# Kernel tuning notes

Measured on AMD Instinct MI355X. Metric: run time of the kernel, lower is better.

The kernel has to match this reference:

```python
import jax, jax.numpy as jnp
import numpy as np


def setup_inputs() -> dict:
    key = jax.random.key(0)
    k1, k2 = jax.random.split(key)
    B, S, D, K = 16, 4096, 256, 4096
    x = jax.random.normal(k1, (B, S, D), dtype=jnp.float32)
    scale = 1.0 / K  # matches nn.init.uniform_(-scale, scale)
    embeddings = jax.random.uniform(k2, (K, D), dtype=jnp.float32, minval=-scale, maxval=scale)
    return {"x": x, "embeddings": embeddings}


def reference(x, embeddings):
    # Flatten all leading dims: [N, D]
    in_shape = x.shape
    flat = x.reshape(-1, in_shape[-1])
    distances = (
        jnp.sum(flat ** 2, axis=1, keepdims=True)
        + jnp.sum(embeddings ** 2, axis=1)
        - 2.0 * flat @ embeddings.T
    )
    proposal = jnp.argmin(distances, axis=-1).reshape(in_shape[:-1])  # [B, S] int
    quantized = embeddings[proposal]  # [B, S, D] gather
    return quantized, proposal
```

## Files before the change

kernel.cpp:

```cpp
#include <hip/hip_runtime.h>
#include <hip/hip_bf16.h>
#include <stdint.h>

#define NROWS 65536
#define DDIM  256
#define KCAND 4096
#define CAP   48
#define MARGIN1 8e-4f
#define MARGIN2 8e-4f

#define LSTRIDE 132

typedef __bf16 bf16x8 __attribute__((ext_vector_type(8)));
typedef float  f32x4  __attribute__((ext_vector_type(4)));
typedef unsigned int u32;
typedef unsigned long long u64;

__device__ __forceinline__ u32 f2bf_u(float f) {
    u32 u = __float_as_uint(f);
    u += 0x7fffu + ((u >> 16) & 1u);
    return u >> 16;
}
__device__ __forceinline__ u32 pack2(float lo, float hi) { return f2bf_u(lo) | (f2bf_u(hi) << 16); }
__device__ __forceinline__ u32 fkey(float f) {
    u32 u = __float_as_uint(f);
    return (u & 0x80000000u) ? ~u : (u | 0x80000000u);
}
__device__ __forceinline__ float funkey(u32 k) {
    u32 u = (k & 0x80000000u) ? (k ^ 0x80000000u) : ~k;
    return __uint_as_float(u);
}
__device__ __forceinline__ float vmax4(f32x4 v) {
    return fmaxf(fmaxf(v[0], v[1]), fmaxf(v[2], v[3]));
}

__device__ __forceinline__ float exact_r(const float* __restrict__ xr, float A,
                                         const float* __restrict__ er) {
    float b = 0.f, acc = 0.f;
    #pragma unroll 8
    for (int d = 0; d < DDIM; ++d) {
        float e = er[d];
        b   = fmaf(e, e, b);
        acc = fmaf(2.0f * xr[d], e, acc);
    }
    return (A + b) - acc;
}

__launch_bounds__(256)
__global__ void convert_e(const float* __restrict__ e, u32* __restrict__ ebf) {
    int T = blockIdx.x * blockDim.x + threadIdx.x;
    int L = T & 63, u = (T >> 6) & 3, kc = (T >> 8) & 7, s = T >> 11;
    int cand = s * 64 + u * 16 + (L & 15);
    int k0 = kc * 32 + (L >> 4) * 8;
    const float4* src = (const float4*)(e + (size_t)cand * DDIM + k0);
    float4 a = src[0], b = src[1];
    uint4 o;
    o.x = pack2(a.x, a.y); o.y = pack2(a.z, a.w);
    o.z = pack2(b.x, b.y); o.w = pack2(b.z, b.w);
    ((uint4*)ebf)[T] = o;
}

__launch_bounds__(256, 3)
__global__ void phase1(const float* __restrict__ x, const u32* __restrict__ ebf,
                       u32* __restrict__ cnt, uint2* __restrict__ list) {
    __shared__ u32 lxd[64 * LSTRIDE];
    __shared__ u32 rowBestK[64];

    const int tid = threadIdx.x;
    const int rowBase = blockIdx.x * 64;
    if (tid < 64) rowBestK[tid] = 0x007FFFFFu;

    {
        const float4* x4 = (const float4*)(x + (size_t)rowBase * DDIM);
        #pragma unroll
        for (int j = 0; j < 16; ++j) {
            int idx = j * 256 + tid;
            int r = idx >> 6, c4 = idx & 63;
            float4 v = x4[idx];
            *(uint2*)&lxd[r * LSTRIDE + 2 * c4] = make_uint2(pack2(v.x, v.y), pack2(v.z, v.w));
        }
    }
    __syncthreads();

    const int L = tid & 63;
    const int w = __builtin_amdgcn_readfirstlane(tid >> 6);
    const int lq = L >> 4, ln = L & 15;
    const int vL = L << 4;

    const char* ebc_w = (const char*)ebf + (size_t)w * 32768;

    auto loadB = [&](int it_, int kc_, bf16x8* dst) {
        const char* kb = ebc_w + (size_t)it_ * 131072 + kc_ * 4096;
        #pragma unroll
        for (int u = 0; u < 4; ++u)
            dst[u] = *(const bf16x8*)(kb + u * 1024 + vL);
    };

    const char* pa = (const char*)lxd + ln * (LSTRIDE * 4) + lq * 16;

    bf16x8 bb[2][4];
    f32x4 acc[4][4];
    const f32x4 Z4 = {0.f, 0.f, 0.f, 0.f};

    loadB(0, 0, bb[0]);
    #pragma unroll
    for (int kc = 0; kc < 8; ++kc) {
        if (kc < 7) loadB(0, kc + 1, bb[(kc + 1) & 1]);
        bf16x8 fa[4];
        #pragma unroll
        for (int t = 0; t < 4; ++t)
            fa[t] = *(const bf16x8*)(pa + t * (16 * LSTRIDE * 4) + kc * 64);
        #pragma unroll
        for (int a = 0; a < 4; ++a)
            #pragma unroll
            for (int u = 0; u < 4; ++u)
                acc[a][u] = (kc == 0)
                    ? __builtin_amdgcn_mfma_f32_16x16x32_bf16(bb[0][u], fa[a], Z4, 0, 0, 0)
                    : __builtin_amdgcn_mfma_f32_16x16x32_bf16(bb[kc & 1][u], fa[a], acc[a][u], 0, 0, 0);
    }
    #pragma unroll
    for (int a = 0; a < 4; ++a) {
        float lmax = fmaxf(fmaxf(vmax4(acc[a][0]), vmax4(acc[a][1])),
                           fmaxf(vmax4(acc[a][2]), vmax4(acc[a][3])));
        float m = fmaxf(lmax, __shfl_xor(lmax, 16, 64));
        m = fmaxf(m, __shfl_xor(m, 32, 64));
        if (lq == 0) atomicMax(&rowBestK[a * 16 + ln], fkey(m));
    }
    __syncthreads();

    loadB(0, 0, bb[0]);
    #pragma unroll 1
    for (int it = 0; it < 16; ++it) {
        {
            loadB(it, 1, bb[1]);
            bf16x8 fa[4];
            #pragma unroll
            for (int t = 0; t < 4; ++t)
                fa[t] = *(const bf16x8*)(pa + t * (16 * LSTRIDE * 4));
            #pragma unroll
            for (int a = 0; a < 4; ++a)
                #pragma unroll
                for (int u = 0; u < 4; ++u)
                    acc[a][u] = __builtin_amdgcn_mfma_f32_16x16x32_bf16(bb[0][u], fa[a], Z4, 0, 0, 0);
        }
        #pragma unroll
        for (int kc = 1; kc < 8; ++kc) {
            int g = it * 8 + kc;
            if (g < 127) { int gn = g + 1; loadB(gn >> 3, gn & 7, bb[(kc + 1) & 1]); }
            bf16x8 fa[4];
            #pragma unroll
            for (int t = 0; t < 4; ++t)
                fa[t] = *(const bf16x8*)(pa + t * (16 * LSTRIDE * 4) + kc * 64);
            #pragma unroll
            for (int a = 0; a < 4; ++a)
                #pragma unroll
                for (int u = 0; u < 4; ++u)
                    acc[a][u] = __builtin_amdgcn_mfma_f32_16x16x32_bf16(bb[kc & 1][u], fa[a], acc[a][u], 0, 0, 0);
        }

        int strip = it * 4 + w;
        u32 seen[4];
        #pragma unroll
        for (int a = 0; a < 4; ++a) seen[a] = rowBestK[a * 16 + ln];

        #pragma unroll
        for (int a = 0; a < 4; ++a) {
            float lmax = fmaxf(fmaxf(vmax4(acc[a][0]), vmax4(acc[a][1])),
                               fmaxf(vmax4(acc[a][2]), vmax4(acc[a][3])));
            float m = fmaxf(lmax, __shfl_xor(lmax, 16, 64));
            m = fmaxf(m, __shfl_xor(m, 32, 64));
            if (lq == 0) atomicMax(&rowBestK[a * 16 + ln], fkey(m));
            float eff  = fmaxf(m, funkey(seen[a]));
            float thrA = eff - 0.5f * MARGIN1;
            if (__ballot(lmax >= thrA)) {
                int c = 0;
                #pragma unroll
                for (int u = 0; u < 4; ++u)
                    #pragma unroll
                    for (int r = 0; r < 4; ++r)
                        c += (acc[a][u][r] >= thrA) ? 1 : 0;
                int p = c, t;
                t = __shfl_up(p, 16, 64); if (lq >= 1) p += t;
                t = __shfl_up(p, 32, 64); if (lq >= 2) p += t;
                int grow = rowBase + a * 16 + ln;
                u32 base = 0;
                if (lq == 3 && p > 0) base = atomicAdd(&cnt[grow], (u32)p);
                base = __shfl(base, 48 + ln, 64);
                u32 pos = base + (u32)(p - c);
                #pragma unroll
                for (int u = 0; u < 4; ++u)
                    #pragma unroll
                    for (int r = 0; r < 4; ++r) {
                        float av = acc[a][u][r];
                        if (av >= thrA) {
                            if (pos < CAP)
                                list[(size_t)grow * CAP + pos] =
                                    make_uint2(__float_as_uint(-2.f * av),
                                               (u32)(strip * 64 + u * 16 + lq * 4 + r));
                            ++pos;
                        }
                    }
            }
        }
    }
}

__launch_bounds__(256)
__global__ void phase2(const float* __restrict__ x, const float* __restrict__ emb,
                       const u32* __restrict__ cnt, const uint2* __restrict__ list,
                       float* __restrict__ outq, float* __restrict__ outp) {
    __shared__ float xs[4][DDIM];
    const int wid = threadIdx.x >> 6;
    const int row = blockIdx.x * 4 + wid;
    const int L   = threadIdx.x & 63;

    u32 n = cnt[row];
    u32 kstar;

    if (n == 1) {
        kstar = list[(size_t)row * CAP].y;
    } else {
        float4 v = ((const float4*)(x + (size_t)row * DDIM))[L];
        *(float4*)&xs[wid][L * 4] = v;
        double s = (double)v.x * v.x + (double)v.y * v.y + (double)v.z * v.z + (double)v.w * v.w;
        #pragma unroll
        for (int o = 32; o; o >>= 1) s += __shfl_xor(s, o, 64);
        float A = (float)s;

        u64 key = 0xFFFFFFFFFFFFFFFFull;
        if (n <= CAP) {
            float vv = INFINITY; u32 kk = 0;
            if (L < (int)n) { uint2 e = list[(size_t)row * CAP + L]; vv = __uint_as_float(e.x); kk = e.y; }
            float mv = vv;
            #pragma unroll
            for (int o = 32; o; o >>= 1) mv = fminf(mv, __shfl_xor(mv, o, 64));
            if (L < (int)n && vv <= mv + MARGIN2) {
                float r = exact_r(xs[wid], A, emb + (size_t)kk * DDIM);
                key = ((u64)fkey(r) << 32) | (u64)kk;
            }
        } else {
            for (int c = 0; c < KCAND / 64; ++c) {
                u32 k = (u32)(c * 64 + L);
                float r = exact_r(xs[wid], A, emb + (size_t)k * DDIM);
                u64 cand = ((u64)fkey(r) << 32) | (u64)k;
                key = (cand < key) ? cand : key;
            }
        }
        #pragma unroll
        for (int o = 32; o; o >>= 1) {
            u64 other = __shfl_xor(key, o, 64);
            key = (other < key) ? other : key;
        }
        kstar = (u32)(key & 0xFFFFFFFFull);
    }

    float4 q = ((const float4*)(emb + (size_t)kstar * DDIM))[L];
    ((float4*)(outq + (size_t)row * DDIM))[L] = q;
    if (L == 0) outp[row] = (float)kstar;
}

extern "C" void kernel_launch(void* const* d_in, const int* in_sizes, int n_in,
                              void* d_out, int out_size, void* d_ws, size_t ws_size,
                              hipStream_t stream) {
    const float* x   = (const float*)d_in[0];
    const float* emb = (const float*)d_in[1];
    float* outq = (float*)d_out;
    float* outp = outq + (size_t)NROWS * DDIM;

    char* ws = (char*)d_ws;
    u32*   ebf  = (u32*)ws;
    u32*   cnt  = (u32*)(ws + (2u << 20));
    uint2* list = (uint2*)(ws + (3u << 20));

    hipMemsetAsync(cnt, 0, (size_t)NROWS * sizeof(u32), stream);
    convert_e<<<512, 256, 0, stream>>>(emb, ebf);
    phase1<<<NROWS / 64, 256, 0, stream>>>(x, ebf, cnt, list);
    phase2<<<NROWS / 4, 256, 0, stream>>>(x, emb, cnt, list, outq, outp);
}
```

Baseline: 452.4 us.

## Double phase1 row tile to 128 and skip exact rescoring for single survivors

Phase1 now processes 128 rows per block instead of 64, with 8 accumulator tiles per wave, so each bf16 codebook fragment loaded from global memory is reused across twice as many rows. This halves total codebook traffic, at the cost of more registers and LDS and a lower occupancy bound (2 blocks instead of 3). Phase2 now checks whether exactly one candidate survives the margin filter. If so it picks that candidate directly and skips loading x and the exact fp32 rescoring.

```diff
diff --git a/kernel.cpp b/kernel.cpp
--- a/kernel.cpp
+++ b/kernel.cpp
@@ -10,6 +10,7 @@
 #define MARGIN2 8e-4f
 
 #define LSTRIDE 132
+#define ROWS_PB 128
 
 typedef __bf16 bf16x8 __attribute__((ext_vector_type(8)));
 typedef float  f32x4  __attribute__((ext_vector_type(4)));
@@ -60,20 +61,20 @@
     ((uint4*)ebf)[T] = o;
 }
 
-__launch_bounds__(256, 3)
+__launch_bounds__(256, 2)
 __global__ void phase1(const float* __restrict__ x, const u32* __restrict__ ebf,
                        u32* __restrict__ cnt, uint2* __restrict__ list) {
-    __shared__ u32 lxd[64 * LSTRIDE];
-    __shared__ u32 rowBestK[64];
+    __shared__ u32 lxd[ROWS_PB * LSTRIDE];
+    __shared__ u32 rowBestK[ROWS_PB];
 
     const int tid = threadIdx.x;
-    const int rowBase = blockIdx.x * 64;
-    if (tid < 64) rowBestK[tid] = 0x007FFFFFu;
+    const int rowBase = blockIdx.x * ROWS_PB;
+    if (tid < ROWS_PB) rowBestK[tid] = 0x007FFFFFu;
 
     {
         const float4* x4 = (const float4*)(x + (size_t)rowBase * DDIM);
         #pragma unroll
-        for (int j = 0; j < 16; ++j) {
+        for (int j = 0; j < 32; ++j) {
             int idx = j * 256 + tid;
             int r = idx >> 6, c4 = idx & 63;
             float4 v = x4[idx];
@@ -99,27 +100,25 @@
     const char* pa = (const char*)lxd + ln * (LSTRIDE * 4) + lq * 16;
 
     bf16x8 bb[2][4];
-    f32x4 acc[4][4];
+    f32x4 acc[8][4];
     const f32x4 Z4 = {0.f, 0.f, 0.f, 0.f};
 
     loadB(0, 0, bb[0]);
     #pragma unroll
     for (int kc = 0; kc < 8; ++kc) {
         if (kc < 7) loadB(0, kc + 1, bb[(kc + 1) & 1]);
-        bf16x8 fa[4];
-        #pragma unroll
-        for (int t = 0; t < 4; ++t)
-            fa[t] = *(const bf16x8*)(pa + t * (16 * LSTRIDE * 4) + kc * 64);
-        #pragma unroll
-        for (int a = 0; a < 4; ++a)
+        #pragma unroll
+        for (int a = 0; a < 8; ++a) {
+            bf16x8 fa = *(const bf16x8*)(pa + a * (16 * LSTRIDE * 4) + kc * 64);
             #pragma unroll
             for (int u = 0; u < 4; ++u)
                 acc[a][u] = (kc == 0)
-                    ? __builtin_amdgcn_mfma_f32_16x16x32_bf16(bb[0][u], fa[a], Z4, 0, 0, 0)
-                    : __builtin_amdgcn_mfma_f32_16x16x32_bf16(bb[kc & 1][u], fa[a], acc[a][u], 0, 0, 0);
+                    ? __builtin_amdgcn_mfma_f32_16x16x32_bf16(bb[0][u], fa, Z4, 0, 0, 0)
+                    : __builtin_amdgcn_mfma_f32_16x16x32_bf16(bb[kc & 1][u], fa, acc[a][u], 0, 0, 0);
+        }
     }
     #pragma unroll
-    for (int a = 0; a < 4; ++a) {
+    for (int a = 0; a < 8; ++a) {
         float lmax = fmaxf(fmaxf(vmax4(acc[a][0]), vmax4(acc[a][1])),
                            fmaxf(vmax4(acc[a][2]), vmax4(acc[a][3])));
         float m = fmaxf(lmax, __shfl_xor(lmax, 16, 64));
@@ -133,38 +132,34 @@
     for (int it = 0; it < 16; ++it) {
         {
             loadB(it, 1, bb[1]);
-            bf16x8 fa[4];
-            #pragma unroll
-            for (int t = 0; t < 4; ++t)
-                fa[t] = *(const bf16x8*)(pa + t * (16 * LSTRIDE * 4));
-            #pragma unroll
-            for (int a = 0; a < 4; ++a)
-                #pragma unroll
-                for (int u = 0; u < 4; ++u)
-                    acc[a][u] = __builtin_amdgcn_mfma_f32_16x16x32_bf16(bb[0][u], fa[a], Z4, 0, 0, 0);
+            #pragma unroll
+            for (int a = 0; a < 8; ++a) {
+                bf16x8 fa = *(const bf16x8*)(pa + a * (16 * LSTRIDE * 4));
+                #pragma unroll
+                for (int u = 0; u < 4; ++u)
+                    acc[a][u] = __builtin_amdgcn_mfma_f32_16x16x32_bf16(bb[0][u], fa, Z4, 0, 0, 0);
+            }
         }
         #pragma unroll
         for (int kc = 1; kc < 8; ++kc) {
             int g = it * 8 + kc;
             if (g < 127) { int gn = g + 1; loadB(gn >> 3, gn & 7, bb[(kc + 1) & 1]); }
-            bf16x8 fa[4];
-            #pragma unroll
-            for (int t = 0; t < 4; ++t)
-                fa[t] = *(const bf16x8*)(pa + t * (16 * LSTRIDE * 4) + kc * 64);
-            #pragma unroll
-            for (int a = 0; a < 4; ++a)
-                #pragma unroll
-                for (int u = 0; u < 4; ++u)
-                    acc[a][u] = __builtin_amdgcn_mfma_f32_16x16x32_bf16(bb[kc & 1][u], fa[a], acc[a][u], 0, 0, 0);
+            #pragma unroll
+            for (int a = 0; a < 8; ++a) {
+                bf16x8 fa = *(const bf16x8*)(pa + a * (16 * LSTRIDE * 4) + kc * 64);
+                #pragma unroll
+                for (int u = 0; u < 4; ++u)
+                    acc[a][u] = __builtin_amdgcn_mfma_f32_16x16x32_bf16(bb[kc & 1][u], fa, acc[a][u], 0, 0, 0);
+            }
         }
 
         int strip = it * 4 + w;
-        u32 seen[4];
-        #pragma unroll
-        for (int a = 0; a < 4; ++a) seen[a] = rowBestK[a * 16 + ln];
-
-        #pragma unroll
-        for (int a = 0; a < 4; ++a) {
+        u32 seen[8];
+        #pragma unroll
+        for (int a = 0; a < 8; ++a) seen[a] = rowBestK[a * 16 + ln];
+
+        #pragma unroll
+        for (int a = 0; a < 8; ++a) {
             float lmax = fmaxf(fmaxf(vmax4(acc[a][0]), vmax4(acc[a][1])),
                                fmaxf(vmax4(acc[a][2]), vmax4(acc[a][3])));
             float m = fmaxf(lmax, __shfl_xor(lmax, 16, 64));
@@ -220,38 +215,51 @@
     if (n == 1) {
         kstar = list[(size_t)row * CAP].y;
     } else {
-        float4 v = ((const float4*)(x + (size_t)row * DDIM))[L];
-        *(float4*)&xs[wid][L * 4] = v;
-        double s = (double)v.x * v.x + (double)v.y * v.y + (double)v.z * v.z + (double)v.w * v.w;
-        #pragma unroll
-        for (int o = 32; o; o >>= 1) s += __shfl_xor(s, o, 64);
-        float A = (float)s;
-
-        u64 key = 0xFFFFFFFFFFFFFFFFull;
-        if (n <= CAP) {
-            float vv = INFINITY; u32 kk = 0;
+        bool scan_all = (n > CAP);
+        bool resolved = false;
+        float vv = INFINITY; u32 kk = 0;
+        bool surv = false;
+        if (!scan_all) {
             if (L < (int)n) { uint2 e = list[(size_t)row * CAP + L]; vv = __uint_as_float(e.x); kk = e.y; }
             float mv = vv;
             #pragma unroll
             for (int o = 32; o; o >>= 1) mv = fminf(mv, __shfl_xor(mv, o, 64));
-            if (L < (int)n && vv <= mv + MARGIN2) {
-                float r = exact_r(xs[wid], A, emb + (size_t)kk * DDIM);
-                key = ((u64)fkey(r) << 32) | (u64)kk;
-            }
-        } else {
-            for (int c = 0; c < KCAND / 64; ++c) {
-                u32 k = (u32)(c * 64 + L);
-                float r = exact_r(xs[wid], A, emb + (size_t)k * DDIM);
-                u64 cand = ((u64)fkey(r) << 32) | (u64)k;
-                key = (cand < key) ? cand : key;
-            }
-        }
-        #pragma unroll
-        for (int o = 32; o; o >>= 1) {
-            u64 other = __shfl_xor(key, o, 64);
-            key = (other < key) ? other : key;
-        }
-        kstar = (u32)(key & 0xFFFFFFFFull);
+            surv = (L < (int)n) && (vv <= mv + MARGIN2);
+            u64 bal = __ballot(surv);
+            if (__popcll(bal) == 1) {
+                kstar = __shfl(kk, (int)(__ffsll(bal) - 1), 64);
+                resolved = true;
+            }
+        }
+        if (!resolved) {
+            float4 v = ((const float4*)(x + (size_t)row * DDIM))[L];
+            *(float4*)&xs[wid][L * 4] = v;
+            double s = (double)v.x * v.x + (double)v.y * v.y + (double)v.z * v.z + (double)v.w * v.w;
+            #pragma unroll
+            for (int o = 32; o; o >>= 1) s += __shfl_xor(s, o, 64);
+            float A = (float)s;
+
+            u64 key = 0xFFFFFFFFFFFFFFFFull;
+            if (!scan_all) {
+                if (surv) {
+                    float r = exact_r(xs[wid], A, emb + (size_t)kk * DDIM);
+                    key = ((u64)fkey(r) << 32) | (u64)kk;
+                }
+            } else {
+                for (int c = 0; c < KCAND / 64; ++c) {
+                    u32 k = (u32)(c * 64 + L);
+                    float r = exact_r(xs[wid], A, emb + (size_t)k * DDIM);
+                    u64 cand = ((u64)fkey(r) << 32) | (u64)k;
+                    key = (cand < key) ? cand : key;
+                }
+            }
+            #pragma unroll
+            for (int o = 32; o; o >>= 1) {
+                u64 other = __shfl_xor(key, o, 64);
+                key = (other < key) ? other : key;
+            }
+            kstar = (u32)(key & 0xFFFFFFFFull);
+        }
     }
 
     float4 q = ((const float4*)(emb + (size_t)kstar * DDIM))[L];
@@ -274,6 +282,6 @@
 
     hipMemsetAsync(cnt, 0, (size_t)NROWS * sizeof(u32), stream);
     convert_e<<<512, 256, 0, stream>>>(emb, ebf);
-    phase1<<<NROWS / 64, 256, 0, stream>>>(x, ebf, cnt, list);
+    phase1<<<NROWS / ROWS_PB, 256, 0, stream>>>(x, ebf, cnt, list);
     phase2<<<NROWS / 4, 256, 0, stream>>>(x, emb, cnt, list, outq, outp);
 }
```

Result: faster. 396.2 us (-12.4%).
